# Kernel optimization log

Hardware: AMD Instinct MI355X
Metric: run time of the kernel (lower is better)

Reference implementation:

```python
import jax, jax.numpy as jnp
import numpy as np

N_NODES = 50000
N_EDGES = 800000
H, D_IN, D_OUT = 4, 256, 64


def setup_inputs() -> dict:
    key = jax.random.key(0)
    ks = jax.random.split(key, 7)
    x = jax.random.normal(ks[0], (N_NODES, D_IN), dtype=jnp.float32)
    idx = jax.random.randint(ks[1], (2, N_EDGES), 0, N_NODES, dtype=jnp.int32)
    elem = jax.random.uniform(ks[2], (N_EDGES,), dtype=jnp.float32)
    Ws = jax.random.normal(ks[3], (H, D_IN, D_OUT), dtype=jnp.float32) * 0.05
    bs = jax.random.normal(ks[4], (H, D_OUT), dtype=jnp.float32) * 0.05
    aw = jax.random.normal(ks[5], (H, 2 * D_OUT + 1), dtype=jnp.float32) * 0.05
    ab = jax.random.normal(ks[6], (H,), dtype=jnp.float32) * 0.05
    return {"x": x, "idx": idx, "elem": elem, "Ws": Ws, "bs": bs, "aw": aw, "ab": ab}


def reference(x, idx, elem, Ws, bs, aw, ab):
    N = x.shape[0]
    O = Ws.shape[-1]
    # per-head MLP (num_mlp_layers=1 -> single Linear): [H, N, O]
    feats = jnp.einsum('nd,hdo->hno', x, Ws) + bs[:, None, :]
    # attention linear on concat(src, dst, elem): split weights instead of
    # materializing the [E, 2O+1] concat; math is identical.
    aw_src, aw_dst, aw_e = aw[:, :O], aw[:, O:2 * O], aw[:, 2 * O]
    a_s = jnp.einsum('hno,ho->hn', feats, aw_src)   # [H, N]
    a_d = jnp.einsum('hno,ho->hn', feats, aw_dst)   # [H, N]
    src, dst = idx[0], idx[1]
    score = a_s[:, src] + a_d[:, dst] + aw_e[:, None] * elem[None, :] + ab[:, None]
    w = jnp.exp(-jax.nn.relu(score / 20.0))        # [H, E], in (0, 1]
    dst_f = feats[:, dst]                          # [H, E, O] gather
    seg = lambda vals: jax.ops.segment_sum(vals, src, num_segments=N)
    pooled = jax.vmap(lambda wi, fi: seg(wi[:, None] * fi))(w, dst_f)  # [H, N, O]
    row_sum = jax.vmap(lambda wi: seg(wi))(w)                          # [H, N]
    out = pooled / row_sum[:, :, None]
    # concat heads along feature dim: [N, H*O]
    return jnp.transpose(out, (1, 0, 2)).reshape(N, H * O)
```

## Files before the change

kernel.cpp:

```cpp
#include <hip/hip_runtime.h>
#include <math.h>

constexpr int DIN = 256;
constexpr int H   = 4;
constexpr int O   = 64;
constexpr int HO  = H * O;
constexpr int AWS = 2 * O + 1;

typedef __bf16 bf16x8 __attribute__((ext_vector_type(8)));
typedef __bf16 bf16x4 __attribute__((ext_vector_type(4)));
typedef float  f32x4  __attribute__((ext_vector_type(4)));

__device__ __forceinline__ float bf2f(unsigned short u) {
    union { unsigned int i; float f; } c;
    c.i = ((unsigned int)u) << 16;
    return c.f;
}

__global__ __launch_bounds__(256) void k_prep(const float* __restrict__ Ws,
    __bf16* __restrict__ Bt, int* __restrict__ cnt, int N)
{
    const int b = blockIdx.x;
    if (b < 256) {
        const int i = b * 256 + threadIdx.x;
        const int k = i & 255;
        const int n = i >> 8;
        Bt[n * 256 + k] = (__bf16)Ws[(n >> 6) * (DIN * O) + k * O + (n & 63)];
    } else {
        const int i = (b - 256) * 256 + threadIdx.x;
        if (i < N) cnt[i] = 0;
    }
}

__global__ __launch_bounds__(256) void k_gemm_hist(const float* __restrict__ x,
    const __bf16* __restrict__ Bt, const float* __restrict__ bs,
    const float* __restrict__ aw, int N, int GB,
    __bf16* __restrict__ F, float* __restrict__ a_sT, float* __restrict__ a_dT,
    const int* __restrict__ idx, int E, int* __restrict__ cnt,
    int* __restrict__ rank)
{
    __shared__ __bf16 As[64][DIN + 8];
    const int b = blockIdx.x;
    const int t = threadIdx.x;

    if (b >= GB) {
        const int base_e = (b - GB) * 1024 + t;
        #pragma unroll
        for (int i = 0; i < 4; ++i) {
            const int e = base_e + i * 256;
            if (e < E) rank[e] = atomicAdd(&cnt[idx[e]], 1);
        }
        return;
    }

    const int w    = t >> 6;
    const int lane = t & 63;
    const int c15  = lane & 15;
    const int quad = lane >> 4;
    const int n0   = b * 64;

    #pragma unroll
    for (int i = 0; i < 16; ++i) {
        const int r   = i * 4 + w;
        const int row = n0 + r;
        float4 xv = make_float4(0.f, 0.f, 0.f, 0.f);
        if (row < N) xv = *(const float4*)&x[(size_t)row * DIN + lane * 4];
        bf16x4 pv = { (__bf16)xv.x, (__bf16)xv.y, (__bf16)xv.z, (__bf16)xv.w };
        *(bf16x4*)&As[r][lane * 4] = pv;
    }
    __syncthreads();

    f32x4 acc[4][4] = {};
    const __bf16* BtW = Bt + (size_t)(w * 64) * 256;
    const int kq = quad * 8;

    #pragma unroll
    for (int k0 = 0; k0 < DIN; k0 += 32) {
        bf16x8 afr[4], bfr[4];
        #pragma unroll
        for (int rt = 0; rt < 4; ++rt)
            afr[rt] = *(const bf16x8*)&As[rt * 16 + c15][k0 + kq];
        #pragma unroll
        for (int ct = 0; ct < 4; ++ct)
            bfr[ct] = *(const bf16x8*)&BtW[(size_t)(ct * 16 + c15) * 256 + k0 + kq];
        #pragma unroll
        for (int rt = 0; rt < 4; ++rt)
            #pragma unroll
            for (int ct = 0; ct < 4; ++ct)
                acc[rt][ct] = __builtin_amdgcn_mfma_f32_16x16x32_bf16(
                    afr[rt], bfr[ct], acc[rt][ct], 0, 0, 0);
    }

    const int h = w;
    float bsv[4], awsv[4], awdv[4];
    #pragma unroll
    for (int ct = 0; ct < 4; ++ct) {
        const int col = ct * 16 + c15;
        bsv[ct]  = bs[w * 64 + col];
        awsv[ct] = aw[h * AWS + col];
        awdv[ct] = aw[h * AWS + O + col];
    }

    #pragma unroll
    for (int rt = 0; rt < 4; ++rt) {
        float psum[4] = {0.f, 0.f, 0.f, 0.f};
        float pdum[4] = {0.f, 0.f, 0.f, 0.f};
        #pragma unroll
        for (int ct = 0; ct < 4; ++ct) {
            #pragma unroll
            for (int reg = 0; reg < 4; ++reg) {
                const float f = acc[rt][ct][reg] + bsv[ct];
                const int row = n0 + rt * 16 + quad * 4 + reg;
                if (row < N)
                    F[(size_t)row * HO + w * 64 + ct * 16 + c15] = (__bf16)f;
                psum[reg] = fmaf(f, awsv[ct], psum[reg]);
                pdum[reg] = fmaf(f, awdv[ct], pdum[reg]);
            }
        }
        #pragma unroll
        for (int reg = 0; reg < 4; ++reg) {
            float v = psum[reg], u = pdum[reg];
            #pragma unroll
            for (int off = 1; off < 16; off <<= 1) {
                v += __shfl_xor(v, off, 64);
                u += __shfl_xor(u, off, 64);
            }
            const int row = n0 + rt * 16 + quad * 4 + reg;
            if (c15 == 0 && row < N) {
                a_sT[row * H + h] = v;
                a_dT[row * H + h] = u;
            }
        }
    }
}

__global__ __launch_bounds__(256) void k_scan1(const int* __restrict__ cnt,
    int* __restrict__ row_ptr, int* __restrict__ bsum, int N)
{
    __shared__ int wsum[4], woff[4];
    const int t = threadIdx.x, b = blockIdx.x;
    const int i = b * 256 + t;
    const int lane = t & 63, w = t >> 6;

    const int v = (i < N) ? cnt[i] : 0;
    int s = v;
    #pragma unroll
    for (int off = 1; off < 64; off <<= 1) {
        int u = __shfl_up(s, off, 64);
        if (lane >= off) s += u;
    }
    if (lane == 63) wsum[w] = s;
    __syncthreads();
    if (t == 0) {
        int run = 0;
        #pragma unroll
        for (int j = 0; j < 4; ++j) { woff[j] = run; run += wsum[j]; }
        bsum[b] = run;
    }
    __syncthreads();
    const int excl = s - v + woff[w];
    if (i < N) row_ptr[i] = excl;
    if (i == N - 1) row_ptr[N] = excl + v;
}

__global__ __launch_bounds__(256) void k_scan2(int* __restrict__ bsum, int nb)
{
    __shared__ int wsum[4], woff[4];
    const int t = threadIdx.x;
    const int lane = t & 63, w = t >> 6;

    const int v = (t < nb) ? bsum[t] : 0;
    int s = v;
    #pragma unroll
    for (int off = 1; off < 64; off <<= 1) {
        int u = __shfl_up(s, off, 64);
        if (lane >= off) s += u;
    }
    if (lane == 63) wsum[w] = s;
    __syncthreads();
    if (t == 0) {
        int run = 0;
        #pragma unroll
        for (int j = 0; j < 4; ++j) { woff[j] = run; run += wsum[j]; }
    }
    __syncthreads();
    const int excl = s - v + woff[w];
    __syncthreads();
    if (t < nb) bsum[t] = excl;
    if (t == 0) bsum[nb] = woff[3] + wsum[3];
}

__global__ __launch_bounds__(256) void k_scatter(const int* __restrict__ idx,
    const float* __restrict__ elem, const int* __restrict__ rank,
    const int* __restrict__ row_ptr, const int* __restrict__ bsum, int E,
    int2* __restrict__ csr)
{
    int e = blockIdx.x * 256 + threadIdx.x;
    if (e >= E) return;
    const int s = idx[e];
    const int d = idx[E + e];
    const int pos = row_ptr[s] + bsum[s >> 8] + rank[e];
    csr[pos] = make_int2(d, __float_as_int(elem[e]));
}

__global__ __launch_bounds__(256) void k_gather(const int* __restrict__ row_ptr,
    const int* __restrict__ bsum, const int2* __restrict__ csr,
    const float* __restrict__ a_sT, const float* __restrict__ a_dT,
    const float* __restrict__ aw, const float* __restrict__ ab,
    const __bf16* __restrict__ F, float* __restrict__ out, int N)
{
    __shared__ int2  s_rec[4][64];
    __shared__ float s_w[4][256];

    const int t    = threadIdx.x;
    const int wv   = t >> 6;
    const int lane = t & 63;
    const int n    = blockIdx.x * 4 + wv;
    if (n >= N) return;
    const int h16  = lane >> 4;

    const int beg = row_ptr[n]     + bsum[n >> 8];
    const int end = row_ptr[n + 1] + bsum[(n + 1) >> 8];

    const float4 as4 = *(const float4*)&a_sT[n * 4];
    const float4 ab4 = *(const float4*)&ab[0];
    const float4 awe4 = make_float4(aw[0 * AWS + 2 * O], aw[1 * AWS + 2 * O],
                                    aw[2 * AWS + 2 * O], aw[3 * AWS + 2 * O]);

    float4 acc = make_float4(0.f, 0.f, 0.f, 0.f);
    float  rs  = 0.f;
    const __bf16* __restrict__ Fl = F + lane * 4;

    for (int base = beg; base < end; base += 64) {
        const int cnt = min(64, end - base);
        if (lane < cnt) {
            const int2 r = csr[base + lane];
            s_rec[wv][lane] = r;
            const float el = __int_as_float(r.y);
            const float4 ad = *(const float4*)&a_dT[r.x * 4];
            float4 w4;
            w4.x = __expf(-fmaxf((as4.x + ad.x + awe4.x * el + ab4.x) * 0.05f, 0.f));
            w4.y = __expf(-fmaxf((as4.y + ad.y + awe4.y * el + ab4.y) * 0.05f, 0.f));
            w4.z = __expf(-fmaxf((as4.z + ad.z + awe4.z * el + ab4.z) * 0.05f, 0.f));
            w4.w = __expf(-fmaxf((as4.w + ad.w + awe4.w * el + ab4.w) * 0.05f, 0.f));
            *(float4*)&s_w[wv][lane * 4] = w4;
        }
        __threadfence_block();

        int j = 0;
        for (; j + 4 <= cnt; j += 4) {
            const int d0 = s_rec[wv][j + 0].x;
            const int d1 = s_rec[wv][j + 1].x;
            const int d2 = s_rec[wv][j + 2].x;
            const int d3 = s_rec[wv][j + 3].x;
            const float w0 = s_w[wv][(j + 0) * 4 + h16];
            const float w1 = s_w[wv][(j + 1) * 4 + h16];
            const float w2 = s_w[wv][(j + 2) * 4 + h16];
            const float w3 = s_w[wv][(j + 3) * 4 + h16];
            const ushort4 f0 = *(const ushort4*)&Fl[(size_t)d0 * HO];
            const ushort4 f1 = *(const ushort4*)&Fl[(size_t)d1 * HO];
            const ushort4 f2 = *(const ushort4*)&Fl[(size_t)d2 * HO];
            const ushort4 f3 = *(const ushort4*)&Fl[(size_t)d3 * HO];
            acc.x = fmaf(w0, bf2f(f0.x), acc.x);
            acc.y = fmaf(w0, bf2f(f0.y), acc.y);
            acc.z = fmaf(w0, bf2f(f0.z), acc.z);
            acc.w = fmaf(w0, bf2f(f0.w), acc.w);
            acc.x = fmaf(w1, bf2f(f1.x), acc.x);
            acc.y = fmaf(w1, bf2f(f1.y), acc.y);
            acc.z = fmaf(w1, bf2f(f1.z), acc.z);
            acc.w = fmaf(w1, bf2f(f1.w), acc.w);
            acc.x = fmaf(w2, bf2f(f2.x), acc.x);
            acc.y = fmaf(w2, bf2f(f2.y), acc.y);
            acc.z = fmaf(w2, bf2f(f2.z), acc.z);
            acc.w = fmaf(w2, bf2f(f2.w), acc.w);
            acc.x = fmaf(w3, bf2f(f3.x), acc.x);
            acc.y = fmaf(w3, bf2f(f3.y), acc.y);
            acc.z = fmaf(w3, bf2f(f3.z), acc.z);
            acc.w = fmaf(w3, bf2f(f3.w), acc.w);
            rs += w0 + w1 + w2 + w3;
        }
        for (; j < cnt; ++j) {
            const int d = s_rec[wv][j].x;
            const float w = s_w[wv][j * 4 + h16];
            const ushort4 fv = *(const ushort4*)&Fl[(size_t)d * HO];
            acc.x = fmaf(w, bf2f(fv.x), acc.x);
            acc.y = fmaf(w, bf2f(fv.y), acc.y);
            acc.z = fmaf(w, bf2f(fv.z), acc.z);
            acc.w = fmaf(w, bf2f(fv.w), acc.w);
            rs += w;
        }
    }

    const float inv = 1.f / rs;
    float4 o = make_float4(acc.x * inv, acc.y * inv, acc.z * inv, acc.w * inv);
    *(float4*)&out[(size_t)n * HO + lane * 4] = o;
}

extern "C" void kernel_launch(void* const* d_in, const int* in_sizes, int n_in,
                              void* d_out, int out_size, void* d_ws, size_t ws_size,
                              hipStream_t stream)
{
    const float* x    = (const float*)d_in[0];
    const int*   idx  = (const int*)d_in[1];
    const float* elem = (const float*)d_in[2];
    const float* Ws   = (const float*)d_in[3];
    const float* bs   = (const float*)d_in[4];
    const float* aw   = (const float*)d_in[5];
    const float* ab   = (const float*)d_in[6];

    const int N = in_sizes[0] / DIN;
    const int E = in_sizes[1] / 2;
    const int nb = (N + 255) / 256;
    const int GB = (N + 63) / 64;
    const int HB = (E + 1023) / 1024;

    __bf16* F      = (__bf16*)d_ws;
    float* a_sT    = (float*)(F + (size_t)N * HO);
    float* a_dT    = a_sT + (size_t)N * H;
    int*   cnt     = (int*)(a_dT + (size_t)N * H);
    int*   row_ptr = cnt + N;
    int*   rank    = row_ptr + (N + 1);
    int*   bsum    = rank + E;
    size_t off = (size_t)((char*)(bsum + nb + 1) - (char*)d_ws);
    off = (off + 7) & ~(size_t)7;
    int2*  csr     = (int2*)((char*)d_ws + off);
    __bf16* Bt     = (__bf16*)(csr + E);
    float* out     = (float*)d_out;

    k_prep<<<256 + nb, 256, 0, stream>>>(Ws, Bt, cnt, N);
    k_gemm_hist<<<GB + HB, 256, 0, stream>>>(x, Bt, bs, aw, N, GB,
                                             F, a_sT, a_dT, idx, E, cnt, rank);
    k_scan1<<<nb, 256, 0, stream>>>(cnt, row_ptr, bsum, N);
    k_scan2<<<1, 256, 0, stream>>>(bsum, nb);
    k_scatter<<<(E + 255) / 256, 256, 0, stream>>>(idx, elem, rank, row_ptr,
                                                   bsum, E, csr);
    k_gather<<<(N + 3) / 4, 256, 0, stream>>>(row_ptr, bsum, csr, a_sT, a_dT,
                                              aw, ab, F, out, N);
}
```

Baseline: 251.3 us.

## Split histogram from GEMM and load A fragments directly from global memory

The fused GEMM+histogram kernel becomes two kernels: a standalone atomic histogram launched first, then the GEMM. The GEMM no longer stages x into shared memory with a barrier. Each wave loads its A fragments straight from global fp32 and converts them to bf16 in registers. This removes LDS traffic and the sync, but each of the 4 waves now re-reads the same x rows from global memory, relying on cache, and the histogram no longer overlaps with the GEMM.

```diff
diff --git a/kernel.cpp b/kernel.cpp
--- a/kernel.cpp
+++ b/kernel.cpp
@@ -8,7 +8,6 @@
 constexpr int AWS = 2 * O + 1;
 
 typedef __bf16 bf16x8 __attribute__((ext_vector_type(8)));
-typedef __bf16 bf16x4 __attribute__((ext_vector_type(4)));
 typedef float  f32x4  __attribute__((ext_vector_type(4)));
 
 __device__ __forceinline__ float bf2f(unsigned short u) {
@@ -32,54 +31,50 @@
     }
 }
 
-__global__ __launch_bounds__(256) void k_gemm_hist(const float* __restrict__ x,
+__global__ __launch_bounds__(256) void k_hist(const int* __restrict__ idx, int E,
+    int* __restrict__ cnt, int* __restrict__ rank)
+{
+    const int e = blockIdx.x * 256 + threadIdx.x;
+    if (e < E) rank[e] = atomicAdd(&cnt[idx[e]], 1);
+}
+
+__global__ __launch_bounds__(256) void k_gemm(const float* __restrict__ x,
     const __bf16* __restrict__ Bt, const float* __restrict__ bs,
-    const float* __restrict__ aw, int N, int GB,
-    __bf16* __restrict__ F, float* __restrict__ a_sT, float* __restrict__ a_dT,
-    const int* __restrict__ idx, int E, int* __restrict__ cnt,
-    int* __restrict__ rank)
-{
-    __shared__ __bf16 As[64][DIN + 8];
-    const int b = blockIdx.x;
-    const int t = threadIdx.x;
-
-    if (b >= GB) {
-        const int base_e = (b - GB) * 1024 + t;
-        #pragma unroll
-        for (int i = 0; i < 4; ++i) {
-            const int e = base_e + i * 256;
-            if (e < E) rank[e] = atomicAdd(&cnt[idx[e]], 1);
-        }
-        return;
-    }
-
+    const float* __restrict__ aw, int N,
+    __bf16* __restrict__ F, float* __restrict__ a_sT, float* __restrict__ a_dT)
+{
+    const int t    = threadIdx.x;
     const int w    = t >> 6;
     const int lane = t & 63;
     const int c15  = lane & 15;
     const int quad = lane >> 4;
-    const int n0   = b * 64;
-
-    #pragma unroll
-    for (int i = 0; i < 16; ++i) {
-        const int r   = i * 4 + w;
-        const int row = n0 + r;
-        float4 xv = make_float4(0.f, 0.f, 0.f, 0.f);
-        if (row < N) xv = *(const float4*)&x[(size_t)row * DIN + lane * 4];
-        bf16x4 pv = { (__bf16)xv.x, (__bf16)xv.y, (__bf16)xv.z, (__bf16)xv.w };
-        *(bf16x4*)&As[r][lane * 4] = pv;
-    }
-    __syncthreads();
+    const int n0   = blockIdx.x * 64;
+    const int kq   = quad * 8;
 
     f32x4 acc[4][4] = {};
     const __bf16* BtW = Bt + (size_t)(w * 64) * 256;
-    const int kq = quad * 8;
+
+    const bool full = (n0 + 64 <= N);
 
     #pragma unroll
     for (int k0 = 0; k0 < DIN; k0 += 32) {
         bf16x8 afr[4], bfr[4];
         #pragma unroll
-        for (int rt = 0; rt < 4; ++rt)
-            afr[rt] = *(const bf16x8*)&As[rt * 16 + c15][k0 + kq];
+        for (int rt = 0; rt < 4; ++rt) {
+            const int row = n0 + rt * 16 + c15;
+            float4 x0 = make_float4(0.f, 0.f, 0.f, 0.f), x1 = x0;
+            if (full || row < N) {
+                const float* xp = &x[(size_t)row * DIN + k0 + kq];
+                x0 = *(const float4*)xp;
+                x1 = *(const float4*)(xp + 4);
+            }
+            bf16x8 a;
+            a[0] = (__bf16)x0.x; a[1] = (__bf16)x0.y;
+            a[2] = (__bf16)x0.z; a[3] = (__bf16)x0.w;
+            a[4] = (__bf16)x1.x; a[5] = (__bf16)x1.y;
+            a[6] = (__bf16)x1.z; a[7] = (__bf16)x1.w;
+            afr[rt] = a;
+        }
         #pragma unroll
         for (int ct = 0; ct < 4; ++ct)
             bfr[ct] = *(const bf16x8*)&BtW[(size_t)(ct * 16 + c15) * 256 + k0 + kq];
@@ -311,8 +306,6 @@
     const int N = in_sizes[0] / DIN;
     const int E = in_sizes[1] / 2;
     const int nb = (N + 255) / 256;
-    const int GB = (N + 63) / 64;
-    const int HB = (E + 1023) / 1024;
 
     __bf16* F      = (__bf16*)d_ws;
     float* a_sT    = (float*)(F + (size_t)N * HO);
@@ -328,8 +321,8 @@
     float* out     = (float*)d_out;
 
     k_prep<<<256 + nb, 256, 0, stream>>>(Ws, Bt, cnt, N);
-    k_gemm_hist<<<GB + HB, 256, 0, stream>>>(x, Bt, bs, aw, N, GB,
-                                             F, a_sT, a_dT, idx, E, cnt, rank);
+    k_hist<<<(E + 255) / 256, 256, 0, stream>>>(idx, E, cnt, rank);
+    k_gemm<<<(N + 63) / 64, 256, 0, stream>>>(x, Bt, bs, aw, N, F, a_sT, a_dT);
     k_scan1<<<nb, 256, 0, stream>>>(cnt, row_ptr, bsum, N);
     k_scan2<<<1, 256, 0, stream>>>(bsum, nb);
     k_scatter<<<(E + 255) / 256, 256, 0, stream>>>(idx, elem, rank, row_ptr,
```

New measurement: 291.6 us. 1.16x slower.
